# Kernel optimization log

Hardware: AMD Instinct MI355X
Metric: run time of the kernel (lower is better)

The kernel has to match this reference:

```python
import jax, jax.numpy as jnp
import numpy as np

EPS = 1e-5

def _layernorm(x, g, b):
    mu = jnp.mean(x, axis=-1, keepdims=True)
    var = jnp.mean(jnp.square(x - mu), axis=-1, keepdims=True)
    return (x - mu) * jax.lax.rsqrt(var + EPS) * g + b

def setup_inputs() -> dict:
    key = jax.random.key(0)
    ks = jax.random.split(key, 12)
    B, S, D, F = 2, 2048, 1024, 4096
    w = lambda k, shp: jax.random.normal(k, shp, dtype=jnp.float32) * 0.02
    return {
        "x":  jax.random.normal(ks[0], (B, S, D), dtype=jnp.float32),
        "Wq": w(ks[1], (D, D)), "bq": jnp.zeros((D,), jnp.float32),
        "Wk": w(ks[2], (D, D)), "bk": jnp.zeros((D,), jnp.float32),
        "Wv": w(ks[3], (D, D)), "bv": jnp.zeros((D,), jnp.float32),
        "W1": w(ks[4], (F, D)), "b1": jnp.zeros((F,), jnp.float32),
        "W2": w(ks[5], (D, F)), "b2": jnp.zeros((D,), jnp.float32),
        "g1": jnp.ones((D,), jnp.float32), "beta1": jnp.zeros((D,), jnp.float32),
        "g2": jnp.ones((D,), jnp.float32), "beta2": jnp.zeros((D,), jnp.float32),
    }

def reference(x, Wq, bq, Wk, bk, Wv, bv, W1, b1, W2, b2, g1, beta1, g2, beta2):
    B, S, D = x.shape
    H = 16
    dk = D // H
    # QKV projections (torch nn.Linear: y = x @ W.T + b)
    q = (x @ Wq.T + bq).reshape(B, S, H, dk).transpose(0, 2, 1, 3)  # [B,H,S,dk]
    k = (x @ Wk.T + bk).reshape(B, S, H, dk).transpose(0, 2, 1, 3)
    v = (x @ Wv.T + bv).reshape(B, S, H, dk).transpose(0, 2, 1, 3)
    # naive full attention (no mask, dropout=identity in eval)
    scores = jnp.einsum("bhqd,bhkd->bhqk", q, k) / jnp.sqrt(jnp.float32(dk))
    probs = jax.nn.softmax(scores, axis=-1)
    attn = jnp.einsum("bhqk,bhkd->bhqd", probs, v)  # [B,H,S,dk]
    attn_out = attn.transpose(0, 2, 1, 3).reshape(B, S, D)  # NOTE: no output proj (combine unused in source)
    # residual + LN1
    h = _layernorm(x + attn_out, g1, beta1)
    # FFN: linear2(relu(linear1(h)))
    ffn = jax.nn.relu(h @ W1.T + b1) @ W2.T + b2
    # residual + LN2
    return _layernorm(h + ffn, g2, beta2)
```

## Files before the change

kernel.cpp:

```cpp
#include <hip/hip_runtime.h>
#include <stdint.h>

typedef unsigned short u16;
typedef __bf16 bf16x8 __attribute__((ext_vector_type(8)));
typedef short s16x8 __attribute__((ext_vector_type(8)));
typedef float f32x4 __attribute__((ext_vector_type(4)));

union FragU { s16x8 s; bf16x8 b; uint4 u; };

__device__ __forceinline__ f32x4 mfma_bf16(s16x8 a, s16x8 b, f32x4 c) {
    FragU ua, ub; ua.s = a; ub.s = b;
    return __builtin_amdgcn_mfma_f32_16x16x32_bf16(ua.b, ub.b, c, 0, 0, 0);
}

__device__ __forceinline__ u16 f2bf(float f) {
    uint32_t u = __float_as_uint(f);
    u += 0x7fffu + ((u >> 16) & 1u);
    return (u16)(u >> 16);
}

__device__ __forceinline__ float bf2f(u16 u) {
    return __uint_as_float((uint32_t)u << 16);
}

__device__ __forceinline__ void gload_lds16(const void* g, void* l) {
    __builtin_amdgcn_global_load_lds((__attribute__((address_space(1))) void*)g,
                                     (__attribute__((address_space(3))) void*)l,
                                     16, 0, 0);
}

__device__ __forceinline__ void xcd_swz(int& bx, int& by, int& bz) {
    int nx = gridDim.x, ny = gridDim.y;
    int nwg = nx * ny * gridDim.z;
    int lin = blockIdx.x + nx * (blockIdx.y + ny * blockIdx.z);
    int cpx = nwg >> 3;
    int s = (lin & 7) * cpx + (lin >> 3);
    bx = s % nx; s /= nx;
    by = s % ny; bz = s / ny;
}

__global__ void k_cast_all(
    const float* __restrict__ s0, u16* __restrict__ d0, int n0,
    const float* __restrict__ s1, u16* __restrict__ d1, int n1,
    const float* __restrict__ s2, u16* __restrict__ d2, int n2,
    const float* __restrict__ s3, u16* __restrict__ d3, int n3,
    const float* __restrict__ s4, u16* __restrict__ d4, int n4_,
    const float* __restrict__ s5, u16* __restrict__ d5, int n5)
{
    const float* src; u16* dst; int n4;
    switch (blockIdx.y) {
        case 0: src = s0; dst = d0; n4 = n0; break;
        case 1: src = s1; dst = d1; n4 = n1; break;
        case 2: src = s2; dst = d2; n4 = n2; break;
        case 3: src = s3; dst = d3; n4 = n3; break;
        case 4: src = s4; dst = d4; n4 = n4_; break;
        default: src = s5; dst = d5; n4 = n5; break;
    }
    int i = blockIdx.x * blockDim.x + threadIdx.x;
    int stride = gridDim.x * blockDim.x;
    for (; i < n4; i += stride) {
        float4 v = ((const float4*)src)[i];
        u16 us[4] = {f2bf(v.x), f2bf(v.y), f2bf(v.z), f2bf(v.w)};
        *(uint2*)(dst + (size_t)i * 4) = *(uint2*)us;
    }
}

template<int RELU, int OUTMODE>
__device__ __forceinline__ void gemm_body(
    u16* __restrict__ As, u16* __restrict__ Bs,
    const u16* __restrict__ A, const u16* __restrict__ W,
    const float* __restrict__ bias, void* __restrict__ Cout,
    int M, int N, int K, int row0, int col0, int kbeg, int kend)
{
    const int tid  = threadIdx.x;
    const int wid  = tid >> 6;
    const int lane = tid & 63;
    const int g    = lane >> 4;
    const int cc   = lane & 15;
    const int wr   = wid >> 1;
    const int wc   = wid & 1;

    f32x4 zero = {0.f, 0.f, 0.f, 0.f};
    f32x4 acc[4][4];
#pragma unroll
    for (int i = 0; i < 4; i++)
#pragma unroll
        for (int j = 0; j < 4; j++) acc[i][j] = zero;

    const int srow = tid >> 3;
    const int scol = ((tid & 7) ^ (srow & 7)) * 8;
    const u16* gA0 = A + (size_t)(row0 + srow) * K + scol;
    const u16* gB0 = W + (size_t)(col0 + srow) * K + scol;
    u16* lA0 = &As[wid * 512];
    u16* lB0 = &Bs[wid * 512];

    const int xm = (cc & 7);

    for (int k0 = kbeg; k0 < kend; k0 += 64) {
#pragma unroll
        for (int j = 0; j < 4; j++)
            gload_lds16(gA0 + (size_t)(j * 32) * K + k0, lA0 + j * 2048);
#pragma unroll
        for (int j = 0; j < 4; j++)
            gload_lds16(gB0 + (size_t)(j * 32) * K + k0, lB0 + j * 2048);
        __syncthreads();

#pragma unroll
        for (int h = 0; h < 2; h++) {
            const int slot = ((h * 4 + g) ^ xm) * 8;
            s16x8 af[4], bf[4];
#pragma unroll
            for (int mi = 0; mi < 4; mi++)
                af[mi] = *(const s16x8*)&As[(wr * 64 + mi * 16 + cc) * 64 + slot];
#pragma unroll
            for (int ni = 0; ni < 4; ni++)
                bf[ni] = *(const s16x8*)&Bs[(wc * 64 + ni * 16 + cc) * 64 + slot];
#pragma unroll
            for (int mi = 0; mi < 4; mi++)
#pragma unroll
                for (int ni = 0; ni < 4; ni++)
                    acc[mi][ni] = mfma_bf16(af[mi], bf[ni], acc[mi][ni]);
        }
        __syncthreads();
    }

#pragma unroll
    for (int ni = 0; ni < 4; ni++) {
        int col = col0 + wc * 64 + ni * 16 + cc;
        float bvv = 0.f;
        if (OUTMODE != 2) bvv = bias[col];
        if (OUTMODE == 3) {
            int head = col >> 6, dh = col & 63;
#pragma unroll
            for (int mi = 0; mi < 4; mi++) {
                int row = row0 + wr * 64 + mi * 16 + g * 4;
                int bb = row >> 11, sl = row & 2047;
                u16 us[4];
#pragma unroll
                for (int r = 0; r < 4; r++) us[r] = f2bf(acc[mi][ni][r] + bvv);
                *(uint2*)&((u16*)Cout)[(((size_t)(bb * 16 + head) * 64 + dh) << 11) + sl]
                    = *(uint2*)us;
            }
        } else {
#pragma unroll
            for (int mi = 0; mi < 4; mi++) {
                int row = row0 + wr * 64 + mi * 16 + g * 4;
#pragma unroll
                for (int r = 0; r < 4; r++) {
                    float v = acc[mi][ni][r] + bvv;
                    if (RELU) v = fmaxf(v, 0.f);
                    size_t idx = (size_t)(row + r) * N + col;
                    if (OUTMODE == 0) ((float*)Cout)[idx] = v;
                    else              ((u16*)Cout)[idx] = f2bf(v);
                }
            }
        }
    }
}

#define GEMM_LDS_DECL \
    __shared__ __align__(16) u16 As[128 * 64]; \
    __shared__ __align__(16) u16 Bs[128 * 64];

__global__ __launch_bounds__(256, 4) void k_gemm_qkv(
    const u16* __restrict__ A, const u16* __restrict__ Wq, const u16* __restrict__ Wk,
    const u16* __restrict__ Wv, const float* __restrict__ bq, const float* __restrict__ bk,
    const float* __restrict__ bv, u16* __restrict__ Q, u16* __restrict__ K,
    u16* __restrict__ Vt, int M, int N, int Kd)
{
    GEMM_LDS_DECL
    int bx, by, bz; xcd_swz(bx, by, bz);
    if (bz == 0)
        gemm_body<0, 1>(As, Bs, A, Wq, bq, Q,  M, N, Kd, by * 128, bx * 128, 0, Kd);
    else if (bz == 1)
        gemm_body<0, 1>(As, Bs, A, Wk, bk, K,  M, N, Kd, by * 128, bx * 128, 0, Kd);
    else
        gemm_body<0, 3>(As, Bs, A, Wv, bv, Vt, M, N, Kd, by * 128, bx * 128, 0, Kd);
}

__global__ __launch_bounds__(256, 4) void k_gemm_relu_bf16(
    const u16* __restrict__ A, const u16* __restrict__ W, const float* __restrict__ bias,
    u16* __restrict__ C, int M, int N, int K)
{
    GEMM_LDS_DECL
    int bx, by, bz; xcd_swz(bx, by, bz);
    gemm_body<1, 1>(As, Bs, A, W, bias, C, M, N, K, by * 128, bx * 128, 0, K);
}

__global__ __launch_bounds__(256, 4) void k_gemm_part(
    const u16* __restrict__ A, const u16* __restrict__ W,
    u16* __restrict__ p0, u16* __restrict__ p1, u16* __restrict__ p2, u16* __restrict__ p3,
    int M, int N, int K)
{
    GEMM_LDS_DECL
    int bx, by, bz; xcd_swz(bx, by, bz);
    u16* out = (bz == 0) ? p0 : (bz == 1) ? p1 : (bz == 2) ? p2 : p3;
    gemm_body<0, 2>(As, Bs, A, W, nullptr, out, M, N, K, by * 128, bx * 128, bz * 1024, bz * 1024 + 1024);
}

__global__ __launch_bounds__(512, 4) void k_flash(
    const u16* __restrict__ Q, const u16* __restrict__ Kb,
    const u16* __restrict__ Vt, float* __restrict__ O)
{
    constexpr int S = 2048, Dm = 1024, H = 16;
    constexpr int KVB = 128, NT = S / KVB;
    constexpr float qsc = 0.125f * 1.44269504f;
    int bx, by, bz; xcd_swz(bx, by, bz);
    int qt = bx, h = by, b = bz;
    int tid = threadIdx.x, wid = tid >> 6, lane = tid & 63;
    int g = lane >> 4, cc = lane & 15;

    __shared__ __align__(16) u16 Ks[2][128 * 64];
    __shared__ __align__(16) u16 Vs[64 * 128];

    int q0 = qt * 128 + wid * 16;
    size_t base = (size_t)b * S * Dm + h * 64;

    FragU uq0, uq1, qs0, qs1;
    uq0.s = *(const s16x8*)(Q + base + (size_t)(q0 + cc) * Dm + g * 8);
    uq1.s = *(const s16x8*)(Q + base + (size_t)(q0 + cc) * Dm + 32 + g * 8);
#pragma unroll
    for (int e = 0; e < 8; e++) {
        qs0.b[e] = (__bf16)((float)uq0.b[e] * qsc);
        qs1.b[e] = (__bf16)((float)uq1.b[e] * qsc);
    }
    s16x8 qf0 = qs0.s, qf1 = qs1.s;

    f32x4 minit = {-8.f, -8.f, -8.f, -8.f};
    f32x4 zero = {0.f, 0.f, 0.f, 0.f};
    f32x4 o[4];
#pragma unroll
    for (int t = 0; t < 4; t++) o[t] = zero;
    f32x4 lacc = zero;

    const int krow = tid >> 3;
    const int kcol = ((tid & 7) ^ (krow & 7)) * 8;
    const u16* kSrcBase = Kb + base + (size_t)krow * Dm + kcol;
    const int kOff = wid * 512;

    const int vrow = tid >> 3;
    const int vch  = (tid & 7) * 8;
    const int xmv  = (vrow & 7) << 3;
    const int cb0  = ((vch >> 5) << 5) | (((vch >> 4) & 1) << 2) | (((vch >> 2) & 3) << 3);
    const int cb1  = cb0 + 64;
    const u16* vSrcBase = Vt + (size_t)(b * H + h) * 64 * S + (size_t)vrow * S;
    u16* vq0a = &Vs[(vrow * 128 + cb0) ^ xmv];
    u16* vq0b = &Vs[(vrow * 128 + cb0 + 8) ^ xmv];
    u16* vq1a = &Vs[(vrow * 128 + cb1) ^ xmv];
    u16* vq1b = &Vs[(vrow * 128 + cb1 + 8) ^ xmv];

    const int xm = cc & 7;

    gload_lds16(kSrcBase,                   &Ks[0][kOff]);
    gload_lds16(kSrcBase + (size_t)64 * Dm, &Ks[0][kOff + 4096]);
    __builtin_amdgcn_sched_barrier(0);
    s16x8 vpre0 = *(const s16x8*)(vSrcBase + vch);
    s16x8 vpre1 = *(const s16x8*)(vSrcBase + 64 + vch);
    __builtin_amdgcn_sched_barrier(0);

    for (int it = 0; it < NT; ++it) {
        const int cur = it & 1;
        const int kv0 = it * KVB;

        asm volatile("s_waitcnt vmcnt(2)" ::: "memory");
        __builtin_amdgcn_s_barrier();
        __builtin_amdgcn_sched_barrier(0);

        {
            FragU a0, a1; a0.s = vpre0; a1.s = vpre1;
            *(uint2*)vq0a = make_uint2(a0.u.x, a0.u.y);
            *(uint2*)vq0b = make_uint2(a0.u.z, a0.u.w);
            *(uint2*)vq1a = make_uint2(a1.u.x, a1.u.y);
            *(uint2*)vq1b = make_uint2(a1.u.z, a1.u.w);
        }
        __builtin_amdgcn_sched_barrier(0);
        if (it + 1 < NT) {
            gload_lds16(kSrcBase + (size_t)(kv0 + KVB) * Dm,      &Ks[cur ^ 1][kOff]);
            gload_lds16(kSrcBase + (size_t)(kv0 + KVB + 64) * Dm, &Ks[cur ^ 1][kOff + 4096]);
        }
        __builtin_amdgcn_sched_barrier(0);
        asm volatile("s_waitcnt lgkmcnt(0)" ::: "memory");
        __builtin_amdgcn_s_barrier();
        __builtin_amdgcn_sched_barrier(0);

        const u16* Kc = Ks[cur];
        f32x4 sacc[8];
#pragma unroll
        for (int t = 0; t < 8; t++) sacc[t] = minit;
        __builtin_amdgcn_s_setprio(1);
#pragma unroll
        for (int t = 0; t < 8; t++) {
            const u16* kr = &Kc[(t * 16 + cc) * 64];
            s16x8 kf0 = *(const s16x8*)(kr + ((0 + g) ^ xm) * 8);
            s16x8 kf1 = *(const s16x8*)(kr + ((4 + g) ^ xm) * 8);
            sacc[t] = mfma_bf16(kf0, qf0, sacc[t]);
            sacc[t] = mfma_bf16(kf1, qf1, sacc[t]);
        }
        __builtin_amdgcn_s_setprio(0);

        FragU pb[4];
#pragma unroll
        for (int t = 0; t < 8; t++)
#pragma unroll
            for (int r = 0; r < 4; r++) {
                float pv = __builtin_amdgcn_exp2f(sacc[t][r]);
                lacc[r] += pv;
                pb[t >> 1].b[(t & 1) * 4 + r] = (__bf16)pv;
            }

        __builtin_amdgcn_s_setprio(1);
#pragma unroll
        for (int td = 0; td < 4; td++) {
            const int rb = (td * 16 + cc) * 128;
#pragma unroll
            for (int kk = 0; kk < 4; kk++) {
                s16x8 vf = *(const s16x8*)&Vs[(rb + kk * 32 + g * 8) ^ (xm << 3)];
                o[td] = mfma_bf16(vf, pb[kk].s, o[td]);
            }
        }
        __builtin_amdgcn_s_setprio(0);

        if (it + 1 < NT) {
            vpre0 = *(const s16x8*)(vSrcBase + kv0 + KVB + vch);
            vpre1 = *(const s16x8*)(vSrcBase + kv0 + KVB + 64 + vch);
        }
        __builtin_amdgcn_sched_barrier(0);
    }

    float l_run = (lacc[0] + lacc[1]) + (lacc[2] + lacc[3]);
    l_run += __shfl_xor(l_run, 16, 64);
    l_run += __shfl_xor(l_run, 32, 64);
    float inv = 1.f / l_run;
#pragma unroll
    for (int td = 0; td < 4; td++) {
        float4 st = {o[td][0] * inv, o[td][1] * inv, o[td][2] * inv, o[td][3] * inv};
        *(float4*)&O[(size_t)(b * S + q0 + cc) * Dm + h * 64 + td * 16 + g * 4] = st;
    }
}

__global__ __launch_bounds__(256) void k_ln1(
    const float* __restrict__ A, const float* __restrict__ B,
    const float* __restrict__ gw, const float* __restrict__ bw,
    u16* __restrict__ outb)
{
    constexpr int D = 1024;
    int row = blockIdx.x;
    int t = threadIdx.x;
    int lane = t & 63, wid = t >> 6;
    float4 va = ((const float4*)(A + (size_t)row * D))[t];
    float4 vb = ((const float4*)(B + (size_t)row * D))[t];
    float v0 = va.x + vb.x, v1 = va.y + vb.y, v2 = va.z + vb.z, v3 = va.w + vb.w;
    float sum = v0 + v1 + v2 + v3;
    float sq  = v0 * v0 + v1 * v1 + v2 * v2 + v3 * v3;
#pragma unroll
    for (int off = 1; off < 64; off <<= 1) {
        sum += __shfl_xor(sum, off, 64);
        sq  += __shfl_xor(sq,  off, 64);
    }
    __shared__ float s1[4], s2[4];
    if (lane == 0) { s1[wid] = sum; s2[wid] = sq; }
    __syncthreads();
    sum = s1[0] + s1[1] + s1[2] + s1[3];
    sq  = s2[0] + s2[1] + s2[2] + s2[3];
    float mu  = sum * (1.f / D);
    float var = sq * (1.f / D) - mu * mu;
    float rs  = rsqrtf(var + 1e-5f);
    float4 gv = ((const float4*)gw)[t];
    float4 bv = ((const float4*)bw)[t];
    u16 us[4] = {f2bf((v0 - mu) * rs * gv.x + bv.x),
                 f2bf((v1 - mu) * rs * gv.y + bv.y),
                 f2bf((v2 - mu) * rs * gv.z + bv.z),
                 f2bf((v3 - mu) * rs * gv.w + bv.w)};
    *(uint2*)(outb + (size_t)row * D + t * 4) = *(uint2*)us;
}

__global__ __launch_bounds__(256) void k_ln2(
    const u16* __restrict__ A,
    const u16* __restrict__ p0, const u16* __restrict__ p1,
    const u16* __restrict__ p2, const u16* __restrict__ p3,
    const float* __restrict__ bias,
    const float* __restrict__ gw, const float* __restrict__ bw,
    float* __restrict__ outf)
{
    constexpr int D = 1024;
    int row = blockIdx.x;
    int t = threadIdx.x;
    int lane = t & 63, wid = t >> 6;
    size_t idx = (size_t)row * D + t * 4;
    uint2 ha = *(const uint2*)(A + idx);
    float4 bb = ((const float4*)bias)[t];
    float v0 = bf2f((u16)ha.x)         + bb.x;
    float v1 = bf2f((u16)(ha.x >> 16)) + bb.y;
    float v2 = bf2f((u16)ha.y)         + bb.z;
    float v3 = bf2f((u16)(ha.y >> 16)) + bb.w;
    const u16* ps[4] = {p0, p1, p2, p3};
#pragma unroll
    for (int pi = 0; pi < 4; pi++) {
        uint2 q = *(const uint2*)(ps[pi] + idx);
        v0 += bf2f((u16)q.x);
        v1 += bf2f((u16)(q.x >> 16));
        v2 += bf2f((u16)q.y);
        v3 += bf2f((u16)(q.y >> 16));
    }
    float sum = v0 + v1 + v2 + v3;
    float sq  = v0 * v0 + v1 * v1 + v2 * v2 + v3 * v3;
#pragma unroll
    for (int off = 1; off < 64; off <<= 1) {
        sum += __shfl_xor(sum, off, 64);
        sq  += __shfl_xor(sq,  off, 64);
    }
    __shared__ float s1[4], s2[4];
    if (lane == 0) { s1[wid] = sum; s2[wid] = sq; }
    __syncthreads();
    sum = s1[0] + s1[1] + s1[2] + s1[3];
    sq  = s2[0] + s2[1] + s2[2] + s2[3];
    float mu  = sum * (1.f / D);
    float var = sq * (1.f / D) - mu * mu;
    float rs  = rsqrtf(var + 1e-5f);
    float4 gv = ((const float4*)gw)[t];
    float4 bv = ((const float4*)bw)[t];
    float4 yo = {(v0 - mu) * rs * gv.x + bv.x,
                 (v1 - mu) * rs * gv.y + bv.y,
                 (v2 - mu) * rs * gv.z + bv.z,
                 (v3 - mu) * rs * gv.w + bv.w};
    ((float4*)(outf + (size_t)row * D))[t] = yo;
}

extern "C" void kernel_launch(void* const* d_in, const int* in_sizes, int n_in,
                              void* d_out, int out_size, void* d_ws, size_t ws_size,
                              hipStream_t stream)
{
    constexpr int B = 2, S = 2048, D = 1024, F = 4096, H = 16;
    constexpr int M = B * S;
    const float* x   = (const float*)d_in[0];
    const float* Wq  = (const float*)d_in[1];
    const float* bq  = (const float*)d_in[2];
    const float* Wk  = (const float*)d_in[3];
    const float* bk  = (const float*)d_in[4];
    const float* Wv  = (const float*)d_in[5];
    const float* bv  = (const float*)d_in[6];
    const float* W1  = (const float*)d_in[7];
    const float* b1  = (const float*)d_in[8];
    const float* W2  = (const float*)d_in[9];
    const float* b2  = (const float*)d_in[10];
    const float* g1  = (const float*)d_in[11];
    const float* be1 = (const float*)d_in[12];
    const float* g2  = (const float*)d_in[13];
    const float* be2 = (const float*)d_in[14];
    float* out = (float*)d_out;

    char* ws = (char*)d_ws;
    size_t off = 0;
    auto alloc = [&](size_t bytes) {
        void* p = ws + off;
        off += (bytes + 255) & ~(size_t)255;
        return p;
    };
    u16* xb   = (u16*)alloc((size_t)M * D * 2);
    u16* wqb  = (u16*)alloc((size_t)D * D * 2);
    u16* wkb  = (u16*)alloc((size_t)D * D * 2);
    u16* wvb  = (u16*)alloc((size_t)D * D * 2);
    u16* w1b  = (u16*)alloc((size_t)F * D * 2);
    u16* w2b  = (u16*)alloc((size_t)D * F * 2);
    u16* Qb   = (u16*)alloc((size_t)M * D * 2);
    u16* Kbf  = (u16*)alloc((size_t)M * D * 2);
    u16* Vtb  = (u16*)alloc((size_t)M * D * 2);
    u16* ffn1 = (u16*)alloc((size_t)M * F * 2);
    float* attn = (float*)alloc((size_t)M * D * 4);
    u16* hb     = (u16*)alloc((size_t)M * D * 2);
    u16* p0 = xb;
    u16* p1 = w1b;
    u16* p2 = (u16*)attn;
    u16* p3 = ((u16*)attn) + (size_t)M * D;

    dim3 blk(256);
    k_cast_all<<<dim3(128, 6), blk, 0, stream>>>(
        x,  xb,  M * D / 4,
        Wq, wqb, D * D / 4,
        Wk, wkb, D * D / 4,
        Wv, wvb, D * D / 4,
        W1, w1b, F * D / 4,
        W2, w2b, D * F / 4);

    k_gemm_qkv<<<dim3(D / 128, M / 128, 3), blk, 0, stream>>>(
        xb, wqb, wkb, wvb, bq, bk, bv, Qb, Kbf, Vtb, M, D, D);
    k_flash<<<dim3(S / 128, H, B), dim3(512), 0, stream>>>(Qb, Kbf, Vtb, attn);
    k_ln1<<<dim3(M), blk, 0, stream>>>(x, attn, g1, be1, hb);
    k_gemm_relu_bf16<<<dim3(F / 128, M / 128), blk, 0, stream>>>(hb, w1b, b1, ffn1, M, F, D);
    k_gemm_part<<<dim3(D / 128, M / 128, 4), blk, 0, stream>>>(
        ffn1, w2b, p0, p1, p2, p3, M, D, F);
    k_ln2<<<dim3(M), blk, 0, stream>>>(hb, p0, p1, p2, p3, b2, g2, be2, out);
}
```

Baseline: 189.0 us.

## Double-buffer GEMM LDS tiles to overlap global loads with MFMA compute

The shared GEMM body now uses two LDS buffers. It issues the next K-tile's direct-to-LDS loads before computing on the current tile, waiting with explicit vmcnt counts and raw s_barriers. MFMA sections get raised wave priority via s_setprio. LDS per block doubles to 64 KB, so launch bounds drop from 4 to 2 blocks per CU, trading occupancy for latency hiding within each block.

```diff
diff --git a/kernel.cpp b/kernel.cpp
--- a/kernel.cpp
+++ b/kernel.cpp
@@ -67,7 +67,7 @@
 
 template<int RELU, int OUTMODE>
 __device__ __forceinline__ void gemm_body(
-    u16* __restrict__ As, u16* __restrict__ Bs,
+    u16* __restrict__ AsB, u16* __restrict__ BsB,
     const u16* __restrict__ A, const u16* __restrict__ W,
     const float* __restrict__ bias, void* __restrict__ Cout,
     int M, int N, int K, int row0, int col0, int kbeg, int kend)
@@ -91,37 +91,59 @@
     const int scol = ((tid & 7) ^ (srow & 7)) * 8;
     const u16* gA0 = A + (size_t)(row0 + srow) * K + scol;
     const u16* gB0 = W + (size_t)(col0 + srow) * K + scol;
-    u16* lA0 = &As[wid * 512];
-    u16* lB0 = &Bs[wid * 512];
 
     const int xm = (cc & 7);
 
-    for (int k0 = kbeg; k0 < kend; k0 += 64) {
+    auto stage = [&](int buf, int k0) {
+        u16* lA0 = AsB + buf * 8192 + wid * 512;
+        u16* lB0 = BsB + buf * 8192 + wid * 512;
 #pragma unroll
         for (int j = 0; j < 4; j++)
             gload_lds16(gA0 + (size_t)(j * 32) * K + k0, lA0 + j * 2048);
 #pragma unroll
         for (int j = 0; j < 4; j++)
             gload_lds16(gB0 + (size_t)(j * 32) * K + k0, lB0 + j * 2048);
-        __syncthreads();
-
+    };
+
+    const int nsteps = (kend - kbeg) >> 6;
+    stage(0, kbeg);
+    __builtin_amdgcn_sched_barrier(0);
+
+    for (int step = 0; step < nsteps; ++step) {
+        const int cur = step & 1;
+        if (step + 1 < nsteps) {
+            stage(cur ^ 1, kbeg + (step + 1) * 64);
+            __builtin_amdgcn_sched_barrier(0);
+            asm volatile("s_waitcnt vmcnt(8)" ::: "memory");
+        } else {
+            asm volatile("s_waitcnt vmcnt(0)" ::: "memory");
+        }
+        __builtin_amdgcn_s_barrier();
+        __builtin_amdgcn_sched_barrier(0);
+
+        const u16* Asc = AsB + cur * 8192;
+        const u16* Bsc = BsB + cur * 8192;
 #pragma unroll
         for (int h = 0; h < 2; h++) {
             const int slot = ((h * 4 + g) ^ xm) * 8;
             s16x8 af[4], bf[4];
 #pragma unroll
             for (int mi = 0; mi < 4; mi++)
-                af[mi] = *(const s16x8*)&As[(wr * 64 + mi * 16 + cc) * 64 + slot];
+                af[mi] = *(const s16x8*)&Asc[(wr * 64 + mi * 16 + cc) * 64 + slot];
 #pragma unroll
             for (int ni = 0; ni < 4; ni++)
-                bf[ni] = *(const s16x8*)&Bs[(wc * 64 + ni * 16 + cc) * 64 + slot];
+                bf[ni] = *(const s16x8*)&Bsc[(wc * 64 + ni * 16 + cc) * 64 + slot];
+            __builtin_amdgcn_s_setprio(1);
 #pragma unroll
             for (int mi = 0; mi < 4; mi++)
 #pragma unroll
                 for (int ni = 0; ni < 4; ni++)
                     acc[mi][ni] = mfma_bf16(af[mi], bf[ni], acc[mi][ni]);
-        }
-        __syncthreads();
+            __builtin_amdgcn_s_setprio(0);
+        }
+        __builtin_amdgcn_sched_barrier(0);
+        __builtin_amdgcn_s_barrier();
+        __builtin_amdgcn_sched_barrier(0);
     }
 
 #pragma unroll
@@ -159,10 +181,10 @@
 }
 
 #define GEMM_LDS_DECL \
-    __shared__ __align__(16) u16 As[128 * 64]; \
-    __shared__ __align__(16) u16 Bs[128 * 64];
-
-__global__ __launch_bounds__(256, 4) void k_gemm_qkv(
+    __shared__ __align__(16) u16 As[2][128 * 64]; \
+    __shared__ __align__(16) u16 Bs[2][128 * 64];
+
+__global__ __launch_bounds__(256, 2) void k_gemm_qkv(
     const u16* __restrict__ A, const u16* __restrict__ Wq, const u16* __restrict__ Wk,
     const u16* __restrict__ Wv, const float* __restrict__ bq, const float* __restrict__ bk,
     const float* __restrict__ bv, u16* __restrict__ Q, u16* __restrict__ K,
@@ -171,23 +193,23 @@
     GEMM_LDS_DECL
     int bx, by, bz; xcd_swz(bx, by, bz);
     if (bz == 0)
-        gemm_body<0, 1>(As, Bs, A, Wq, bq, Q,  M, N, Kd, by * 128, bx * 128, 0, Kd);
+        gemm_body<0, 1>(&As[0][0], &Bs[0][0], A, Wq, bq, Q,  M, N, Kd, by * 128, bx * 128, 0, Kd);
     else if (bz == 1)
-        gemm_body<0, 1>(As, Bs, A, Wk, bk, K,  M, N, Kd, by * 128, bx * 128, 0, Kd);
+        gemm_body<0, 1>(&As[0][0], &Bs[0][0], A, Wk, bk, K,  M, N, Kd, by * 128, bx * 128, 0, Kd);
     else
-        gemm_body<0, 3>(As, Bs, A, Wv, bv, Vt, M, N, Kd, by * 128, bx * 128, 0, Kd);
-}
-
-__global__ __launch_bounds__(256, 4) void k_gemm_relu_bf16(
+        gemm_body<0, 3>(&As[0][0], &Bs[0][0], A, Wv, bv, Vt, M, N, Kd, by * 128, bx * 128, 0, Kd);
+}
+
+__global__ __launch_bounds__(256, 2) void k_gemm_relu_bf16(
     const u16* __restrict__ A, const u16* __restrict__ W, const float* __restrict__ bias,
     u16* __restrict__ C, int M, int N, int K)
 {
     GEMM_LDS_DECL
     int bx, by, bz; xcd_swz(bx, by, bz);
-    gemm_body<1, 1>(As, Bs, A, W, bias, C, M, N, K, by * 128, bx * 128, 0, K);
-}
-
-__global__ __launch_bounds__(256, 4) void k_gemm_part(
+    gemm_body<1, 1>(&As[0][0], &Bs[0][0], A, W, bias, C, M, N, K, by * 128, bx * 128, 0, K);
+}
+
+__global__ __launch_bounds__(256, 2) void k_gemm_part(
     const u16* __restrict__ A, const u16* __restrict__ W,
     u16* __restrict__ p0, u16* __restrict__ p1, u16* __restrict__ p2, u16* __restrict__ p3,
     int M, int N, int K)
@@ -195,7 +217,8 @@
     GEMM_LDS_DECL
     int bx, by, bz; xcd_swz(bx, by, bz);
     u16* out = (bz == 0) ? p0 : (bz == 1) ? p1 : (bz == 2) ? p2 : p3;
-    gemm_body<0, 2>(As, Bs, A, W, nullptr, out, M, N, K, by * 128, bx * 128, bz * 1024, bz * 1024 + 1024);
+    gemm_body<0, 2>(&As[0][0], &Bs[0][0], A, W, nullptr, out, M, N, K, by * 128, bx * 128,
+                    bz * 1024, bz * 1024 + 1024);
 }
 
 __global__ __launch_bounds__(512, 4) void k_flash(
```

Result: slower. 204.3 us (+8.1%).
